# Performance work log

Measured on AMD Instinct MI355X. Metric: run time of the kernel, lower is better.

Reference implementation:

```python
import jax, jax.numpy as jnp
import numpy as np

N = 4_000_000
EPS = 1e-6

# Quaternion layout: (w, x, y, z)

def _qmul(q1, q2):
    w1, v1 = q1[..., :1], q1[..., 1:]
    w2, v2 = q2[..., :1], q2[..., 1:]
    w = w1 * w2 - jnp.sum(v1 * v2, axis=-1, keepdims=True)
    v = w1 * v2 + w2 * v1 + jnp.cross(v1, v2)
    return jnp.concatenate([w, v], axis=-1)

def _qinv(q):
    # unit quaternion inverse = conjugate
    return q * jnp.array([1.0, -1.0, -1.0, -1.0], dtype=q.dtype)

def _qlog(q):
    # SO(3) log map: returns tangent vector theta * axis, shape [..., 3]
    w, v = q[..., 0], q[..., 1:]
    nv = jnp.linalg.norm(v, axis=-1)
    small = nv < EPS
    nv_safe = jnp.where(small, 1.0, nv)
    theta = 2.0 * jnp.arctan2(nv, w)
    # small-angle limit: theta/nv -> 2/w
    scale = jnp.where(small, 2.0 / w, theta / nv_safe)
    return v * scale[..., None]

def setup_inputs() -> dict:
    key = jax.random.key(0)
    k1, k2 = jax.random.split(key)
    a = jax.random.normal(k1, (N, 4), dtype=jnp.float32)
    a = a / jnp.linalg.norm(a, axis=-1, keepdims=True)
    idd = jax.random.normal(k2, (N, 4), dtype=jnp.float32)
    idd = idd / jnp.linalg.norm(idd, axis=-1, keepdims=True)
    return {"a": a, "idd": idd}

def reference(a, idd):
    # (a.Inv() @ idd).Log().norm()
    rel = _qmul(_qinv(a), idd)          # [N,4] relative rotation
    tangent = _qlog(rel)                 # [N,3] log map
    return jnp.linalg.norm(tangent)      # scalar Frobenius norm
```

## Files before the change

kernel.cpp:

```cpp
#include <hip/hip_runtime.h>
#include <math.h>

#define BLOCK 256
#define UNROLL 8
#define TILE (BLOCK * UNROLL)

__device__ __forceinline__ float theta_sq(float4 qa, float4 qb) {
    float w1 = qa.x, x1 = -qa.y, y1 = -qa.z, z1 = -qa.w;
    float w2 = qb.x, x2 = qb.y,  y2 = qb.z,  z2 = qb.w;
    float w  = w1*w2 - (x1*x2 + y1*y2 + z1*z2);
    float vx = w1*x2 + w2*x1 + (y1*z2 - z1*y2);
    float vy = w1*y2 + w2*y1 + (z1*x2 - x1*z2);
    float vz = w1*z2 + w2*z1 + (x1*y2 - y1*x2);
    float nv2 = vx*vx + vy*vy + vz*vz;
    float nv  = sqrtf(nv2);
    if (nv < 1e-6f) {
        float s = 2.0f / w;
        return nv2 * s * s;
    }
    float rn = rsqrtf(w*w + nv2);
    float c  = w * rn;
    float ac = fabsf(c);
    float p  = ((-0.0187293f*ac + 0.0742610f)*ac - 0.2121144f)*ac + 1.5707288f;
    float r  = sqrtf(fmaxf(1.0f - ac, 0.0f)) * p;
    float acosc = (c >= 0.0f) ? r : (3.14159265358979f - r);
    float theta = 2.0f * acosc;
    return theta * theta;
}

__global__ __launch_bounds__(BLOCK) void geo_loss_kernel(
        const float4* __restrict__ a,
        const float4* __restrict__ idd,
        float* __restrict__ ws, int n) {
    const int tid  = threadIdx.x;
    const int base = blockIdx.x * TILE + tid;
    float acc = 0.0f;

    if (base + (UNROLL - 1) * BLOCK < n) {
        float4 qa[UNROLL], qb[UNROLL];
        #pragma unroll
        for (int k = 0; k < UNROLL; k++) qa[k] = a[base + k * BLOCK];
        #pragma unroll
        for (int k = 0; k < UNROLL; k++) qb[k] = idd[base + k * BLOCK];
        #pragma unroll
        for (int k = 0; k < UNROLL; k++) acc += theta_sq(qa[k], qb[k]);
    } else {
        for (int k = 0; k < UNROLL; k++) {
            int idx = base + k * BLOCK;
            if (idx < n) acc += theta_sq(a[idx], idd[idx]);
        }
    }

    #pragma unroll
    for (int off = 32; off > 0; off >>= 1)
        acc += __shfl_down(acc, off, 64);
    __shared__ float smem[BLOCK / 64];
    int lane = tid & 63;
    int wid  = tid >> 6;
    if (lane == 0) smem[wid] = acc;
    __syncthreads();
    if (tid == 0) {
        float s = smem[0] + smem[1] + smem[2] + smem[3];
        atomicAdd(ws, s);
    }
}

__global__ void finalize_kernel(const float* __restrict__ ws,
                                float* __restrict__ out) {
    out[0] = sqrtf(ws[0]);
}

extern "C" void kernel_launch(void* const* d_in, const int* in_sizes, int n_in,
                              void* d_out, int out_size, void* d_ws, size_t ws_size,
                              hipStream_t stream) {
    const float4* a   = (const float4*)d_in[0];
    const float4* idd = (const float4*)d_in[1];
    int n = in_sizes[0] / 4;
    float* ws = (float*)d_ws;

    hipMemsetAsync(ws, 0, sizeof(float), stream);

    int grid = (n + TILE - 1) / TILE;
    geo_loss_kernel<<<grid, BLOCK, 0, stream>>>(a, idd, ws, n);
    finalize_kernel<<<1, 1, 0, stream>>>(ws, (float*)d_out);
}
```

Measured before the change: 142.9 us.

## Use per-wave contiguous tiles with nontemporal vector loads and deeper unroll

Each wavefront now owns a contiguous tile of 64*12 quaternions instead of the block striding across a shared tile, and the loop unroll goes from 8 to 12. Loads use __builtin_nontemporal_load on ext_vector float4 so the streamed inputs can bypass cache retention. The aim is more bytes in flight per wave and less cache pollution on a purely bandwidth-bound reduction. Holding 24 float4 values per thread raises register pressure, and the larger tiles mean fewer blocks in the grid.

```diff
diff --git a/kernel.cpp b/kernel.cpp
--- a/kernel.cpp
+++ b/kernel.cpp
@@ -2,10 +2,12 @@
 #include <math.h>
 
 #define BLOCK 256
-#define UNROLL 8
-#define TILE (BLOCK * UNROLL)
+#define UNROLL 12
+#define WTILE (64 * UNROLL)
 
-__device__ __forceinline__ float theta_sq(float4 qa, float4 qb) {
+typedef float vfloat4 __attribute__((ext_vector_type(4)));
+
+__device__ __forceinline__ float theta_sq(vfloat4 qa, vfloat4 qb) {
     float w1 = qa.x, x1 = -qa.y, y1 = -qa.z, z1 = -qa.w;
     float w2 = qb.x, x2 = qb.y,  y2 = qb.z,  z2 = qb.w;
     float w  = w1*w2 - (x1*x2 + y1*y2 + z1*z2);
@@ -29,24 +31,29 @@
 }
 
 __global__ __launch_bounds__(BLOCK) void geo_loss_kernel(
-        const float4* __restrict__ a,
-        const float4* __restrict__ idd,
+        const vfloat4* __restrict__ a,
+        const vfloat4* __restrict__ idd,
         float* __restrict__ ws, int n) {
     const int tid  = threadIdx.x;
-    const int base = blockIdx.x * TILE + tid;
+    const int lane = tid & 63;
+    const int gw   = (blockIdx.x * BLOCK + tid) >> 6;
+    const int wbase = gw * WTILE;
     float acc = 0.0f;
 
-    if (base + (UNROLL - 1) * BLOCK < n) {
-        float4 qa[UNROLL], qb[UNROLL];
+    if (wbase + WTILE <= n) {
+        vfloat4 qa[UNROLL], qb[UNROLL];
         #pragma unroll
-        for (int k = 0; k < UNROLL; k++) qa[k] = a[base + k * BLOCK];
+        for (int k = 0; k < UNROLL; k++)
+            qa[k] = __builtin_nontemporal_load(&a[wbase + k * 64 + lane]);
         #pragma unroll
-        for (int k = 0; k < UNROLL; k++) qb[k] = idd[base + k * BLOCK];
+        for (int k = 0; k < UNROLL; k++)
+            qb[k] = __builtin_nontemporal_load(&idd[wbase + k * 64 + lane]);
         #pragma unroll
-        for (int k = 0; k < UNROLL; k++) acc += theta_sq(qa[k], qb[k]);
-    } else {
+        for (int k = 0; k < UNROLL; k++)
+            acc += theta_sq(qa[k], qb[k]);
+    } else if (wbase < n) {
         for (int k = 0; k < UNROLL; k++) {
-            int idx = base + k * BLOCK;
+            int idx = wbase + k * 64 + lane;
             if (idx < n) acc += theta_sq(a[idx], idd[idx]);
         }
     }
@@ -55,8 +62,7 @@
     for (int off = 32; off > 0; off >>= 1)
         acc += __shfl_down(acc, off, 64);
     __shared__ float smem[BLOCK / 64];
-    int lane = tid & 63;
-    int wid  = tid >> 6;
+    int wid = tid >> 6;
     if (lane == 0) smem[wid] = acc;
     __syncthreads();
     if (tid == 0) {
@@ -73,14 +79,15 @@
 extern "C" void kernel_launch(void* const* d_in, const int* in_sizes, int n_in,
                               void* d_out, int out_size, void* d_ws, size_t ws_size,
                               hipStream_t stream) {
-    const float4* a   = (const float4*)d_in[0];
-    const float4* idd = (const float4*)d_in[1];
+    const vfloat4* a   = (const vfloat4*)d_in[0];
+    const vfloat4* idd = (const vfloat4*)d_in[1];
     int n = in_sizes[0] / 4;
     float* ws = (float*)d_ws;
 
-    hipMemsetAsync(ws, 0, sizeof(float), stream);
+    (void)hipMemsetAsync(ws, 0, sizeof(float), stream);
 
-    int grid = (n + TILE - 1) / TILE;
+    int nwaves = (n + WTILE - 1) / WTILE;
+    int grid   = (nwaves + (BLOCK / 64) - 1) / (BLOCK / 64);
     geo_loss_kernel<<<grid, BLOCK, 0, stream>>>(a, idd, ws, n);
     finalize_kernel<<<1, 1, 0, stream>>>(ws, (float*)d_out);
 }
```

New measurement: 145.5 us. No clear change (+1.8%).

## Replace atomic accumulation with per-block partials and a tree-reduced finalize

Applied to the files above, without the earlier changes.

Each block now writes its partial sum to its own workspace slot instead of atomically adding to a single float, and a 256-thread finalize kernel reduces all partials and takes the square root. This drops the memset launch and the contention on one atomic address. Block size goes from 256 to 512, per-thread unroll from 8 to 4, and launch bounds now request 8 waves per EU. The workspace must hold one float per block, and the summation order becomes deterministic.

```diff
diff --git a/kernel.cpp b/kernel.cpp
--- a/kernel.cpp
+++ b/kernel.cpp
@@ -1,8 +1,8 @@
 #include <hip/hip_runtime.h>
 #include <math.h>
 
-#define BLOCK 256
-#define UNROLL 8
+#define BLOCK 512
+#define UNROLL 4
 #define TILE (BLOCK * UNROLL)
 
 __device__ __forceinline__ float theta_sq(float4 qa, float4 qb) {
@@ -28,10 +28,10 @@
     return theta * theta;
 }
 
-__global__ __launch_bounds__(BLOCK) void geo_loss_kernel(
+__global__ __launch_bounds__(BLOCK, 8) void geo_loss_kernel(
         const float4* __restrict__ a,
         const float4* __restrict__ idd,
-        float* __restrict__ ws, int n) {
+        float* __restrict__ partials, int n) {
     const int tid  = threadIdx.x;
     const int base = blockIdx.x * TILE + tid;
     float acc = 0.0f;
@@ -60,14 +60,29 @@
     if (lane == 0) smem[wid] = acc;
     __syncthreads();
     if (tid == 0) {
-        float s = smem[0] + smem[1] + smem[2] + smem[3];
-        atomicAdd(ws, s);
+        float s = 0.0f;
+        #pragma unroll
+        for (int i = 0; i < BLOCK / 64; i++) s += smem[i];
+        partials[blockIdx.x] = s;
     }
 }
 
-__global__ void finalize_kernel(const float* __restrict__ ws,
-                                float* __restrict__ out) {
-    out[0] = sqrtf(ws[0]);
+__global__ __launch_bounds__(256) void finalize_kernel(
+        const float* __restrict__ partials,
+        float* __restrict__ out, int nparts) {
+    float acc = 0.0f;
+    for (int i = threadIdx.x; i < nparts; i += 256)
+        acc += partials[i];
+    #pragma unroll
+    for (int off = 32; off > 0; off >>= 1)
+        acc += __shfl_down(acc, off, 64);
+    __shared__ float smem[4];
+    int lane = threadIdx.x & 63;
+    int wid  = threadIdx.x >> 6;
+    if (lane == 0) smem[wid] = acc;
+    __syncthreads();
+    if (threadIdx.x == 0)
+        out[0] = sqrtf(smem[0] + smem[1] + smem[2] + smem[3]);
 }
 
 extern "C" void kernel_launch(void* const* d_in, const int* in_sizes, int n_in,
@@ -78,9 +93,7 @@
     int n = in_sizes[0] / 4;
     float* ws = (float*)d_ws;
 
-    hipMemsetAsync(ws, 0, sizeof(float), stream);
-
     int grid = (n + TILE - 1) / TILE;
     geo_loss_kernel<<<grid, BLOCK, 0, stream>>>(a, idd, ws, n);
-    finalize_kernel<<<1, 1, 0, stream>>>(ws, (float*)d_out);
+    finalize_kernel<<<1, 256, 0, stream>>>(ws, (float*)d_out, grid);
 }
```

Measured after the change: 141.7 us. About the same (-0.8%).
